# Performance work log

Hardware: AMD Instinct MI355X
Metric: run time of the kernel (lower is better)

The kernel has to match this reference:

```python
import jax, jax.numpy as jnp
import numpy as np

ALPHA = 1.0


def setup_inputs() -> dict:
    key = jax.random.key(0)
    k1, k2 = jax.random.split(key)
    N, K, D = 131072, 512, 512
    inputs = jax.random.normal(k1, (N, D), dtype=jnp.float32)
    # xavier-uniform style init for clusters
    limit = float(np.sqrt(6.0 / (K + D)))
    clusters = jax.random.uniform(k2, (K, D), dtype=jnp.float32, minval=-limit, maxval=limit)
    return {"inputs": inputs, "clusters": clusters}


def reference(inputs, clusters):
    # (same math as sum((x[:,None,:]-c)**2, -1), without the N x K x D intermediate)
    x2 = jnp.sum(inputs * inputs, axis=1, keepdims=True)          # [N, 1]
    c2 = jnp.sum(clusters * clusters, axis=1)[None, :]            # [1, K]
    d2 = jnp.maximum(x2 + c2 - 2.0 * (inputs @ clusters.T), 0.0)  # [N, K]
    q = 1.0 / (1.0 + d2 / ALPHA)
    q = q ** ((ALPHA + 1.0) / 2.0)
    return q / jnp.sum(q, axis=1, keepdims=True)
```

## Files before the change

### kernel.cpp

```cpp
#include <hip/hip_runtime.h>
#include <hip/hip_bf16.h>
#include <stdint.h>

#define NPTS 131072
#define DIM  512
#define KC   512
#define BM   64
#define BK   32
#define NKT  16

typedef float f32x16 __attribute__((ext_vector_type(16)));
typedef float f32x4  __attribute__((ext_vector_type(4)));
typedef short bf16x8 __attribute__((ext_vector_type(8)));

__device__ __forceinline__ float sq4(f32x4 a) {
  return a.x*a.x + a.y*a.y + a.z*a.z + a.w*a.w;
}

__device__ __forceinline__ bf16x8 pack8c(f32x4 a, f32x4 b) {
  union { __hip_bfloat162 h; short s[2]; } u0, u1, u2, u3;
  u0.h = __float22bfloat162_rn(make_float2(a.x, a.y));
  u1.h = __float22bfloat162_rn(make_float2(a.z, a.w));
  u2.h = __float22bfloat162_rn(make_float2(b.x, b.y));
  u3.h = __float22bfloat162_rn(make_float2(b.z, b.w));
  bf16x8 r;
  r[0] = u0.s[0]; r[1] = u0.s[1]; r[2] = u1.s[0]; r[3] = u1.s[1];
  r[4] = u2.s[0]; r[5] = u2.s[1]; r[6] = u3.s[0]; r[7] = u3.s[1];
  return r;
}

__device__ __forceinline__ short f2bf(float f) {
  union { float f; unsigned u; } v; v.f = f;
  unsigned r = v.u + 0x7FFFu + ((v.u >> 16) & 1u);
  return (short)(r >> 16);
}
__device__ __forceinline__ bf16x8 pack8(f32x4 a, f32x4 b) {
  bf16x8 p;
  p[0] = f2bf(a.x); p[1] = f2bf(a.y); p[2] = f2bf(a.z); p[3] = f2bf(a.w);
  p[4] = f2bf(b.x); p[5] = f2bf(b.y); p[6] = f2bf(b.z); p[7] = f2bf(b.w);
  return p;
}

__device__ __forceinline__ void gload_lds16(const void* g, void* l) {
  __builtin_amdgcn_global_load_lds(
      (const __attribute__((address_space(1))) unsigned int*)g,
      (__attribute__((address_space(3))) unsigned int*)l, 16, 0, 0);
}

__global__ void dec_pack(const float* __restrict__ C, short* __restrict__ Bp,
                         float* __restrict__ c2) {
  const int n    = blockIdx.x;
  const int lane = threadIdx.x;
  const float* src = C + (size_t)n * DIM + lane * 8;
  f32x4 v0 = *(const f32x4*)src;
  f32x4 v1 = *(const f32x4*)(src + 4);
  float s = sq4(v0) + sq4(v1);
  #pragma unroll
  for (int m = 1; m < 64; m <<= 1) s += __shfl_xor(s, m, 64);
  if (lane == 0) c2[n] = s;
  const int kt = lane >> 2;
  const int st = (lane >> 1) & 1;
  const int hh = lane & 1;
  const int wn = n >> 7, nt = (n >> 5) & 3, r = n & 31;
  const size_t slot =
      (((size_t)(kt * 2 + st) * 4 + wn) * 4 + nt) * 64 + hh * 32 + r;
  *(bf16x8*)(Bp + slot * 8) = pack8(v0, v1);
}

__global__ __launch_bounds__(512, 4)
void dec_main(const float* __restrict__ X, const short* __restrict__ Bp,
              const float* __restrict__ c2g, float* __restrict__ out) {
  __shared__ short Bh[3][8192];
  __shared__ float Ab[2][2048];

  const int tid  = threadIdx.x;
  const int lane = tid & 63;
  const int wave = tid >> 6;
  const int wm   = wave >> 2;
  const int wn   = wave & 3;
  const int l31  = lane & 31;
  const int h    = lane >> 5;
  const int row0 = blockIdx.x * BM;

  const float* asrc = X + (size_t)(row0 + (tid >> 3)) * DIM +
                      (((tid & 7) ^ ((tid >> 3) & 7)) << 2);
  const short* bsrc = Bp + tid * 8;

  const int abase = (wm * 32 + l31) * BK;
  const int asw   = l31 & 7;

  f32x16 acc[4];
  #pragma unroll
  for (int nt = 0; nt < 4; ++nt) acc[nt] = (f32x16)0.f;
  float x2 = 0.f;

  gload_lds16(bsrc, &Bh[0][tid * 8]);
  gload_lds16(bsrc + 4096, &Bh[0][4096 + tid * 8]);
  gload_lds16(asrc, &Ab[0][tid * 4]);
  __builtin_amdgcn_sched_barrier(0);
  gload_lds16(bsrc + 8192, &Bh[1][tid * 8]);
  gload_lds16(bsrc + 8192 + 4096, &Bh[1][4096 + tid * 8]);
  __builtin_amdgcn_sched_barrier(0);

  int rb = 0;
  for (int kt = 0; kt < NKT; ++kt) {
    const int rb1 = (rb == 2) ? 0 : rb + 1;
    const int rb2 = (rb == 0) ? 2 : rb - 1;

    asm volatile("s_waitcnt vmcnt(2)" ::: "memory");
    __builtin_amdgcn_sched_barrier(0);
    __builtin_amdgcn_s_barrier();
    __builtin_amdgcn_sched_barrier(0);
    {
      const int q  = (2 * kt + 2 < 32) ? 2 * kt + 2 : 31;
      const int ka = (kt + 1 < NKT) ? kt + 1 : NKT - 1;
      gload_lds16(bsrc + (size_t)q * 8192, &Bh[rb2][tid * 8]);
      gload_lds16(bsrc + (size_t)q * 8192 + 4096, &Bh[rb2][4096 + tid * 8]);
      gload_lds16(asrc + ka * BK, &Ab[(kt + 1) & 1][tid * 4]);
    }
    __builtin_amdgcn_sched_barrier(0);
    {
      const float* A = &Ab[kt & 1][0];
      f32x4 lo = *(const f32x4*)&A[abase + (((h * 2 + 0) ^ asw) << 2)];
      f32x4 hi = *(const f32x4*)&A[abase + (((h * 2 + 1) ^ asw) << 2)];
      x2 += sq4(lo) + sq4(hi);
      bf16x8 af = pack8c(lo, hi);
      bf16x8 bfr[4];
      #pragma unroll
      for (int nt = 0; nt < 4; ++nt)
        bfr[nt] = *(const bf16x8*)&Bh[rb][(wn * 4 + nt) * 512 + lane * 8];
      #pragma unroll
      for (int nt = 0; nt < 4; ++nt)
        acc[nt] = __builtin_amdgcn_mfma_f32_32x32x16_bf16(
            af, bfr[nt], acc[nt], 0, 0, 0);
    }

    asm volatile("s_waitcnt vmcnt(3)" ::: "memory");
    __builtin_amdgcn_sched_barrier(0);
    __builtin_amdgcn_s_barrier();
    __builtin_amdgcn_sched_barrier(0);
    {
      const int q = (2 * kt + 3 < 32) ? 2 * kt + 3 : 31;
      gload_lds16(bsrc + (size_t)q * 8192, &Bh[rb][tid * 8]);
      gload_lds16(bsrc + (size_t)q * 8192 + 4096, &Bh[rb][4096 + tid * 8]);
    }
    __builtin_amdgcn_sched_barrier(0);
    {
      const float* A = &Ab[kt & 1][0];
      f32x4 lo = *(const f32x4*)&A[abase + (((4 + h * 2 + 0) ^ asw) << 2)];
      f32x4 hi = *(const f32x4*)&A[abase + (((4 + h * 2 + 1) ^ asw) << 2)];
      x2 += sq4(lo) + sq4(hi);
      bf16x8 af = pack8c(lo, hi);
      bf16x8 bfr[4];
      #pragma unroll
      for (int nt = 0; nt < 4; ++nt)
        bfr[nt] = *(const bf16x8*)&Bh[rb1][(wn * 4 + nt) * 512 + lane * 8];
      #pragma unroll
      for (int nt = 0; nt < 4; ++nt)
        acc[nt] = __builtin_amdgcn_mfma_f32_32x32x16_bf16(
            af, bfr[nt], acc[nt], 0, 0, 0);
    }

    rb = (rb + 2 >= 3) ? rb - 1 : rb + 2;
  }

  __syncthreads();

  x2 += __shfl_xor(x2, 32, 64);

  float c2v[4];
  #pragma unroll
  for (int nt = 0; nt < 4; ++nt) c2v[nt] = c2g[wn * 128 + nt * 32 + l31];

  float srow[16];
  #pragma unroll
  for (int r = 0; r < 16; ++r) {
    const int mloc = (r & 3) + 8 * (r >> 2) + 4 * h;
    const float x2m = __shfl(x2, mloc, 64);
    float s = 0.f;
    #pragma unroll
    for (int nt = 0; nt < 4; ++nt) {
      float d2 = fmaxf(x2m + c2v[nt] - 2.f * acc[nt][r], 0.f);
      float q = __builtin_amdgcn_rcpf(1.f + d2);
      acc[nt][r] = q;
      s += q;
    }
    #pragma unroll
    for (int msk = 1; msk < 32; msk <<= 1) s += __shfl_xor(s, msk, 64);
    srow[r] = s;
  }

  float* part   = &Ab[0][0];
  float* rowinv = &Ab[0][4 * BM];

  if (l31 == 0) {
    #pragma unroll
    for (int r = 0; r < 16; ++r)
      part[wn * BM + wm * 32 + (r & 3) + 8 * (r >> 2) + 4 * h] = srow[r];
  }
  __syncthreads();
  if (tid < BM)
    rowinv[tid] = __builtin_amdgcn_rcpf(part[tid] + part[BM + tid] +
                                        part[2 * BM + tid] + part[3 * BM + tid]);
  __syncthreads();

  #pragma unroll
  for (int r = 0; r < 16; ++r) {
    const int row = wm * 32 + (r & 3) + 8 * (r >> 2) + 4 * h;
    const float iv = rowinv[row];
    float* o = out + (size_t)(row0 + row) * KC + wn * 128 + l31;
    #pragma unroll
    for (int nt = 0; nt < 4; ++nt)
      o[nt * 32] = acc[nt][r] * iv;
  }
}

extern "C" void kernel_launch(void* const* d_in, const int* in_sizes, int n_in,
                              void* d_out, int out_size, void* d_ws, size_t ws_size,
                              hipStream_t stream) {
  const float* X = (const float*)d_in[0];
  const float* C = (const float*)d_in[1];
  float* out = (float*)d_out;

  short* Bp = (short*)d_ws;
  float* c2 = (float*)((char*)d_ws + (size_t)KC * DIM * 2);

  dec_pack<<<KC, 64, 0, stream>>>(C, Bp, c2);
  dec_main<<<NPTS / BM, 512, 0, stream>>>(X, Bp, c2, out);
}
```

Baseline: 172.3 us.

## Halve block to four waves, each computing two M tiles for B-fragment reuse

```diff
diff --git a/kernel.cpp b/kernel.cpp
--- a/kernel.cpp
+++ b/kernel.cpp
@@ -67,7 +67,7 @@
   *(bf16x8*)(Bp + slot * 8) = pack8(v0, v1);
 }
 
-__global__ __launch_bounds__(512, 4)
+__global__ __launch_bounds__(256, 2)
 void dec_main(const float* __restrict__ X, const short* __restrict__ Bp,
               const float* __restrict__ c2g, float* __restrict__ out) {
   __shared__ short Bh[3][8192];
@@ -75,31 +75,37 @@
 
   const int tid  = threadIdx.x;
   const int lane = tid & 63;
-  const int wave = tid >> 6;
-  const int wm   = wave >> 2;
-  const int wn   = wave & 3;
+  const int wn   = tid >> 6;
   const int l31  = lane & 31;
   const int h    = lane >> 5;
   const int row0 = blockIdx.x * BM;
 
-  const float* asrc = X + (size_t)(row0 + (tid >> 3)) * DIM +
-                      (((tid & 7) ^ ((tid >> 3) & 7)) << 2);
+  const int art = tid >> 3;
+  const int act = tid & 7;
+  const float* asrcL = X + (size_t)(row0 + art) * DIM +
+                       ((act ^ (art & 7)) << 2);
+  const float* asrcH = X + (size_t)(row0 + 32 + art) * DIM +
+                       ((act ^ (art & 7)) << 2);
   const short* bsrc = Bp + tid * 8;
 
-  const int abase = (wm * 32 + l31) * BK;
-  const int asw   = l31 & 7;
-
-  f32x16 acc[4];
-  #pragma unroll
-  for (int nt = 0; nt < 4; ++nt) acc[nt] = (f32x16)0.f;
-  float x2 = 0.f;
-
-  gload_lds16(bsrc, &Bh[0][tid * 8]);
-  gload_lds16(bsrc + 4096, &Bh[0][4096 + tid * 8]);
-  gload_lds16(asrc, &Ab[0][tid * 4]);
+  const int asw = l31 & 7;
+
+  f32x16 acc[2][4];
+  #pragma unroll
+  for (int mt = 0; mt < 2; ++mt)
+    #pragma unroll
+    for (int nt = 0; nt < 4; ++nt) acc[mt][nt] = (f32x16)0.f;
+  float x2s[2] = {0.f, 0.f};
+
+  #pragma unroll
+  for (int sw = 0; sw < 4; ++sw)
+    gload_lds16(bsrc + sw * 2048, &Bh[0][sw * 2048 + tid * 8]);
+  gload_lds16(asrcL, &Ab[0][tid * 4]);
+  gload_lds16(asrcH, &Ab[0][1024 + tid * 4]);
   __builtin_amdgcn_sched_barrier(0);
-  gload_lds16(bsrc + 8192, &Bh[1][tid * 8]);
-  gload_lds16(bsrc + 8192 + 4096, &Bh[1][4096 + tid * 8]);
+  #pragma unroll
+  for (int sw = 0; sw < 4; ++sw)
+    gload_lds16(bsrc + 8192 + sw * 2048, &Bh[1][sw * 2048 + tid * 8]);
   __builtin_amdgcn_sched_barrier(0);
 
   int rb = 0;
@@ -107,58 +113,79 @@
     const int rb1 = (rb == 2) ? 0 : rb + 1;
     const int rb2 = (rb == 0) ? 2 : rb - 1;
 
-    asm volatile("s_waitcnt vmcnt(2)" ::: "memory");
+    asm volatile("s_waitcnt vmcnt(4)" ::: "memory");
     __builtin_amdgcn_sched_barrier(0);
     __builtin_amdgcn_s_barrier();
     __builtin_amdgcn_sched_barrier(0);
     {
       const int q  = (2 * kt + 2 < 32) ? 2 * kt + 2 : 31;
       const int ka = (kt + 1 < NKT) ? kt + 1 : NKT - 1;
-      gload_lds16(bsrc + (size_t)q * 8192, &Bh[rb2][tid * 8]);
-      gload_lds16(bsrc + (size_t)q * 8192 + 4096, &Bh[rb2][4096 + tid * 8]);
-      gload_lds16(asrc + ka * BK, &Ab[(kt + 1) & 1][tid * 4]);
+      #pragma unroll
+      for (int sw = 0; sw < 4; ++sw)
+        gload_lds16(bsrc + (size_t)q * 8192 + sw * 2048,
+                    &Bh[rb2][sw * 2048 + tid * 8]);
+      gload_lds16(asrcL + ka * BK, &Ab[(kt + 1) & 1][tid * 4]);
+      gload_lds16(asrcH + ka * BK, &Ab[(kt + 1) & 1][1024 + tid * 4]);
     }
     __builtin_amdgcn_sched_barrier(0);
     {
       const float* A = &Ab[kt & 1][0];
-      f32x4 lo = *(const f32x4*)&A[abase + (((h * 2 + 0) ^ asw) << 2)];
-      f32x4 hi = *(const f32x4*)&A[abase + (((h * 2 + 1) ^ asw) << 2)];
-      x2 += sq4(lo) + sq4(hi);
-      bf16x8 af = pack8c(lo, hi);
+      bf16x8 af[2];
+      #pragma unroll
+      for (int mt = 0; mt < 2; ++mt) {
+        f32x4 lo = *(const f32x4*)
+            &A[mt * 1024 + l31 * 32 + (((h * 2 + 0) ^ asw) << 2)];
+        f32x4 hi = *(const f32x4*)
+            &A[mt * 1024 + l31 * 32 + (((h * 2 + 1) ^ asw) << 2)];
+        x2s[mt] += sq4(lo) + sq4(hi);
+        af[mt] = pack8c(lo, hi);
+      }
       bf16x8 bfr[4];
       #pragma unroll
       for (int nt = 0; nt < 4; ++nt)
         bfr[nt] = *(const bf16x8*)&Bh[rb][(wn * 4 + nt) * 512 + lane * 8];
       #pragma unroll
-      for (int nt = 0; nt < 4; ++nt)
-        acc[nt] = __builtin_amdgcn_mfma_f32_32x32x16_bf16(
-            af, bfr[nt], acc[nt], 0, 0, 0);
-    }
-
-    asm volatile("s_waitcnt vmcnt(3)" ::: "memory");
+      for (int mt = 0; mt < 2; ++mt)
+        #pragma unroll
+        for (int nt = 0; nt < 4; ++nt)
+          acc[mt][nt] = __builtin_amdgcn_mfma_f32_32x32x16_bf16(
+              af[mt], bfr[nt], acc[mt][nt], 0, 0, 0);
+    }
+
+    asm volatile("s_waitcnt vmcnt(6)" ::: "memory");
     __builtin_amdgcn_sched_barrier(0);
     __builtin_amdgcn_s_barrier();
     __builtin_amdgcn_sched_barrier(0);
     {
       const int q = (2 * kt + 3 < 32) ? 2 * kt + 3 : 31;
-      gload_lds16(bsrc + (size_t)q * 8192, &Bh[rb][tid * 8]);
-      gload_lds16(bsrc + (size_t)q * 8192 + 4096, &Bh[rb][4096 + tid * 8]);
+      #pragma unroll
+      for (int sw = 0; sw < 4; ++sw)
+        gload_lds16(bsrc + (size_t)q * 8192 + sw * 2048,
+                    &Bh[rb][sw * 2048 + tid * 8]);
     }
     __builtin_amdgcn_sched_barrier(0);
     {
       const float* A = &Ab[kt & 1][0];
-      f32x4 lo = *(const f32x4*)&A[abase + (((4 + h * 2 + 0) ^ asw) << 2)];
-      f32x4 hi = *(const f32x4*)&A[abase + (((4 + h * 2 + 1) ^ asw) << 2)];
-      x2 += sq4(lo) + sq4(hi);
-      bf16x8 af = pack8c(lo, hi);
+      bf16x8 af[2];
+      #pragma unroll
+      for (int mt = 0; mt < 2; ++mt) {
+        f32x4 lo = *(const f32x4*)
+            &A[mt * 1024 + l31 * 32 + (((4 + h * 2 + 0) ^ asw) << 2)];
+        f32x4 hi = *(const f32x4*)
+            &A[mt * 1024 + l31 * 32 + (((4 + h * 2 + 1) ^ asw) << 2)];
+        x2s[mt] += sq4(lo) + sq4(hi);
+        af[mt] = pack8c(lo, hi);
+      }
       bf16x8 bfr[4];
       #pragma unroll
       for (int nt = 0; nt < 4; ++nt)
         bfr[nt] = *(const bf16x8*)&Bh[rb1][(wn * 4 + nt) * 512 + lane * 8];
       #pragma unroll
-      for (int nt = 0; nt < 4; ++nt)
-        acc[nt] = __builtin_amdgcn_mfma_f32_32x32x16_bf16(
-            af, bfr[nt], acc[nt], 0, 0, 0);
+      for (int mt = 0; mt < 2; ++mt)
+        #pragma unroll
+        for (int nt = 0; nt < 4; ++nt)
+          acc[mt][nt] = __builtin_amdgcn_mfma_f32_32x32x16_bf16(
+              af[mt], bfr[nt], acc[mt][nt], 0, 0, 0);
     }
 
     rb = (rb + 2 >= 3) ? rb - 1 : rb + 2;
@@ -166,28 +193,32 @@
 
   __syncthreads();
 
-  x2 += __shfl_xor(x2, 32, 64);
+  #pragma unroll
+  for (int mt = 0; mt < 2; ++mt) x2s[mt] += __shfl_xor(x2s[mt], 32, 64);
 
   float c2v[4];
   #pragma unroll
   for (int nt = 0; nt < 4; ++nt) c2v[nt] = c2g[wn * 128 + nt * 32 + l31];
 
-  float srow[16];
-  #pragma unroll
-  for (int r = 0; r < 16; ++r) {
-    const int mloc = (r & 3) + 8 * (r >> 2) + 4 * h;
-    const float x2m = __shfl(x2, mloc, 64);
-    float s = 0.f;
-    #pragma unroll
-    for (int nt = 0; nt < 4; ++nt) {
-      float d2 = fmaxf(x2m + c2v[nt] - 2.f * acc[nt][r], 0.f);
-      float q = __builtin_amdgcn_rcpf(1.f + d2);
-      acc[nt][r] = q;
-      s += q;
-    }
-    #pragma unroll
-    for (int msk = 1; msk < 32; msk <<= 1) s += __shfl_xor(s, msk, 64);
-    srow[r] = s;
+  float srow[2][16];
+  #pragma unroll
+  for (int mt = 0; mt < 2; ++mt) {
+    #pragma unroll
+    for (int r = 0; r < 16; ++r) {
+      const int mloc = (r & 3) + 8 * (r >> 2) + 4 * h;
+      const float x2m = __shfl(x2s[mt], mloc, 64);
+      float s = 0.f;
+      #pragma unroll
+      for (int nt = 0; nt < 4; ++nt) {
+        float d2 = fmaxf(x2m + c2v[nt] - 2.f * acc[mt][nt][r], 0.f);
+        float q = __builtin_amdgcn_rcpf(1.f + d2);
+        acc[mt][nt][r] = q;
+        s += q;
+      }
+      #pragma unroll
+      for (int msk = 1; msk < 32; msk <<= 1) s += __shfl_xor(s, msk, 64);
+      srow[mt][r] = s;
+    }
   }
 
   float* part   = &Ab[0][0];
@@ -195,8 +226,10 @@
 
   if (l31 == 0) {
     #pragma unroll
-    for (int r = 0; r < 16; ++r)
-      part[wn * BM + wm * 32 + (r & 3) + 8 * (r >> 2) + 4 * h] = srow[r];
+    for (int mt = 0; mt < 2; ++mt)
+      #pragma unroll
+      for (int r = 0; r < 16; ++r)
+        part[wn * BM + mt * 32 + (r & 3) + 8 * (r >> 2) + 4 * h] = srow[mt][r];
   }
   __syncthreads();
   if (tid < BM)
@@ -205,13 +238,16 @@
   __syncthreads();
 
   #pragma unroll
-  for (int r = 0; r < 16; ++r) {
-    const int row = wm * 32 + (r & 3) + 8 * (r >> 2) + 4 * h;
-    const float iv = rowinv[row];
-    float* o = out + (size_t)(row0 + row) * KC + wn * 128 + l31;
-    #pragma unroll
-    for (int nt = 0; nt < 4; ++nt)
-      o[nt * 32] = acc[nt][r] * iv;
+  for (int mt = 0; mt < 2; ++mt) {
+    #pragma unroll
+    for (int r = 0; r < 16; ++r) {
+      const int row = mt * 32 + (r & 3) + 8 * (r >> 2) + 4 * h;
+      const float iv = rowinv[row];
+      float* o = out + (size_t)(row0 + row) * KC + wn * 128 + l31;
+      #pragma unroll
+      for (int nt = 0; nt < 4; ++nt)
+        o[nt * 32] = acc[mt][nt][r] * iv;
+    }
   }
 }
 
@@ -226,5 +262,5 @@
   float* c2 = (float*)((char*)d_ws + (size_t)KC * DIM * 2);
 
   dec_pack<<<KC, 64, 0, stream>>>(C, Bp, c2);
-  dec_main<<<NPTS / BM, 512, 0, stream>>>(X, Bp, c2, out);
-}
+  dec_main<<<NPTS / BM, 256, 0, stream>>>(X, Bp, c2, out);
+}
```

After: 173.6 us. No clear change (+0.8%).
